# Optimization experiments

Hardware: AMD Instinct MI355X
Metric: run time of the kernel (lower is better)

Reference implementation:

```python
import jax, jax.numpy as jnp
import numpy as np

N = 20000          # num_node
E = 160000         # num edges (avg degree 8)
IN_N = 64          # in_features_node
IN_E = 32          # in_features_edge
HN = 64            # nhid_node
HE = 64            # nhid_edge
KAPPA = 0.9
ITERS = 8          # fixed Picard iterations for the equilibrium solve


def setup_inputs() -> dict:
    key = jax.random.key(0)
    ks = jax.random.split(key, 16)
    f32 = jnp.float32

    def w(k, shape, fan_in):
        return (jax.random.normal(k, shape, dtype=f32) / np.sqrt(fan_in)).astype(f32)

    return {
        # graph structure (int constants)
        "R": jax.random.randint(ks[0], (E,), 0, N),   # receiver node per edge
        "S": jax.random.randint(ks[1], (E,), 0, N),   # sender node per edge
        "H": jax.random.randint(ks[2], (E,), 0, N),   # edge->node aggregation index
        # features (features-first layout, as in the torch code)
        "node_data": jax.random.normal(ks[3], (IN_N, N), dtype=f32),
        "Ra_data": jax.random.normal(ks[4], (IN_E, E), dtype=f32),
        # INECN_Layer parameters
        "W_es": w(ks[5], (HE, HN), HN),      # sender-message weight
        "W_er": w(ks[6], (HE, HN), HN),      # receiver-message weight
        "Omega_e": w(ks[7], (HE, IN_E), IN_E),
        "Wn": w(ks[8], (HN, HN), HN),        # implicit node-state weight
        "Bm": w(ks[9], (HN, HE), HE),        # edge->node mixing
        "Omega_n": w(ks[10], (HN, IN_N), IN_N),
        # dense head (V_0: nhid->nhid, V_1: nhid->in_features_node)
        "V0_w": w(ks[11], (HN, HN), HN),
        "V0_b": jnp.zeros((HN,), dtype=f32),
        "V1_w": w(ks[12], (IN_N, HN), HN),
        "V1_b": jnp.zeros((IN_N,), dtype=f32),
    }


def reference(R, S, H, node_data, Ra_data, W_es, W_er, Omega_e, Wn, Bm,
              Omega_n, V0_w, V0_b, V1_w, V1_b):
    # spectral-norm style contraction: ||kappa * Wn / ||Wn|||| <= kappa (adj_rho = 1)
    Wn_hat = (KAPPA * Wn) / jnp.maximum(jnp.linalg.norm(Wn), 1.0)

    bias_e = Omega_e @ Ra_data        # [HE, E] injected edge features
    bias_n = Omega_n @ node_data      # [HN, N] injected node features

    def step(X, _):
        # edge update: messages from sender/receiver node states
        He_logits = W_es @ X[:, S] + W_er @ X[:, R] + bias_e      # [HE, E]
        He = jax.nn.relu(He_logits)
        # aggregate edge states back to nodes
        agg = jax.ops.segment_sum(He.T, H, num_segments=N).T      # [HE, N] -> [HE, N]
        # implicit node update (contraction => convergent fixed point)
        X_new = jax.nn.relu(Wn_hat @ X + Bm @ agg + bias_n)       # [HN, N]
        return X_new, None

    X0 = jnp.zeros((HN, N), dtype=node_data.dtype)
    X, _ = jax.lax.scan(step, X0, None, length=ITERS)

    # final edge states / logits at the (approximate) fixed point
    He_logits3 = W_es @ X[:, S] + W_er @ X[:, R] + bias_e         # [HE, E]
    He = jax.nn.relu(He_logits3)

    # dense head: x = V_1(dropout(relu(V_0(x.T))))  (eval mode: dropout = identity)
    x = X.T                                                        # [N, HN]
    x = jax.nn.relu(x @ V0_w.T + V0_b)                             # [N, HN]
    x = x @ V1_w.T + V1_b                                          # [N, IN_N]
    return (x, He, He_logits3)
```

## Files before the change

### kernel.cpp

```cpp
#include <hip/hip_runtime.h>
#include <math.h>

#define KAPPA 0.9f
#define ST 68
#define TN 32

__device__ __forceinline__ float relu_f(float v) { return fmaxf(v, 0.0f); }

__global__ __launch_bounds__(256) void wnhat_kernel(const float* __restrict__ Wn,
                                                    float* __restrict__ Wn_hat) {
  __shared__ float red[4];
  int t = threadIdx.x;
  float v[16];
  float s = 0.f;
#pragma unroll
  for (int j = 0; j < 16; ++j) { v[j] = Wn[t + 256 * j]; s += v[j] * v[j]; }
#pragma unroll
  for (int off = 32; off > 0; off >>= 1) s += __shfl_down(s, off, 64);
  if ((t & 63) == 0) red[t >> 6] = s;
  __syncthreads();
  float norm = sqrtf(red[0] + red[1] + red[2] + red[3]);
  float scale = KAPPA / fmaxf(norm, 1.0f);
#pragma unroll
  for (int j = 0; j < 16; ++j) Wn_hat[t + 256 * j] = v[j] * scale;
}

__global__ __launch_bounds__(256) void bias_n_kernel(const float* __restrict__ node_data,
                                                     const float* __restrict__ Om_n,
                                                     float* __restrict__ bias_n, int N) {
  __shared__ float NdT[64][ST];
  __shared__ float Om[64][ST];
  int t = threadIdx.x;
  int n_base = blockIdx.x * 64;
#pragma unroll
  for (int j = 0; j < 16; ++j) {
    int f = t + 256 * j;
    int r = f >> 6, c = f & 63;
    float val = (n_base + c < N) ? node_data[(size_t)r * N + n_base + c] : 0.f;
    NdT[c][r] = val;
    Om[r][c] = Om_n[f];
  }
  __syncthreads();
  int ni = t & 15, h4 = (t >> 4) * 4;
  float acc[4][4] = {};
#pragma unroll 4
  for (int k = 0; k < 64; k += 4) {
    float4 a[4], w[4];
#pragma unroll
    for (int i = 0; i < 4; ++i) a[i] = *(const float4*)&NdT[ni + 16 * i][k];
#pragma unroll
    for (int j = 0; j < 4; ++j) w[j] = *(const float4*)&Om[h4 + j][k];
#pragma unroll
    for (int i = 0; i < 4; ++i)
#pragma unroll
      for (int j = 0; j < 4; ++j)
        acc[i][j] += a[i].x * w[j].x + a[i].y * w[j].y + a[i].z * w[j].z + a[i].w * w[j].w;
  }
#pragma unroll
  for (int i = 0; i < 4; ++i) {
    int n = n_base + ni + 16 * i;
    if (n < N) {
      float4 o = make_float4(acc[i][0], acc[i][1], acc[i][2], acc[i][3]);
      *(float4*)&bias_n[(size_t)n * 64 + h4] = o;
    }
  }
}

__global__ void hist_kernel(const int* __restrict__ H, int* __restrict__ count, int E) {
  int e = blockIdx.x * 256 + threadIdx.x;
  if (e < E) atomicAdd(&count[H[e]], 1);
}

__global__ __launch_bounds__(256) void scan_kernel(int* count, int* row_off, int* cursor,
                                                   int N, int E) {
  __shared__ int offs[256];
  __shared__ int sums[256];
  int t = threadIdx.x;
  int chunk = (N + 255) / 256;
  int lo = t * chunk, hi = min(lo + chunk, N);
  int s = 0;
  for (int n = lo; n < hi; ++n) s += count[n];
  sums[t] = s;
  __syncthreads();
  if (t == 0) {
    int run = 0;
    for (int i = 0; i < 256; ++i) { offs[i] = run; run += sums[i]; }
  }
  __syncthreads();
  int run = offs[t];
  for (int n = lo; n < hi; ++n) {
    int c = count[n];
    row_off[n] = run;
    cursor[n] = run;
    run += c;
  }
  if (t == 0) row_off[N] = E;
}

__global__ void scatter_kernel(const int* __restrict__ H, const int* __restrict__ S,
                               const int* __restrict__ R, int* cursor,
                               int* __restrict__ Ss, int* __restrict__ Rs,
                               int* __restrict__ inv_perm, int E) {
  int e = blockIdx.x * 256 + threadIdx.x;
  if (e < E) {
    int h = H[e];
    int pos = atomicAdd(&cursor[h], 1);
    Ss[pos] = S[e];
    Rs[pos] = R[e];
    inv_perm[e] = pos;
  }
}

__global__ __launch_bounds__(256) void bias_build_kernel(const float* __restrict__ Ra,
                                                         const float* __restrict__ Om_e,
                                                         const int* __restrict__ inv_perm,
                                                         float* __restrict__ bias_s, int E) {
  __shared__ float OmT[64][36];
  __shared__ float RaT[64][36];
  int t = threadIdx.x;
  int e_base = blockIdx.x * 64;
#pragma unroll
  for (int j = 0; j < 8; ++j) {
    int f = t + 256 * j;
    int r = f >> 5, c = f & 31;
    OmT[r][c] = Om_e[f];
  }
#pragma unroll
  for (int j = 0; j < 8; ++j) {
    int f = t + 256 * j;
    int r = f >> 6, c = f & 63;
    int ee = e_base + c;
    RaT[c][r] = (ee < E) ? Ra[(size_t)r * E + ee] : 0.f;
  }
  __syncthreads();
  int ei = t & 15, h4 = (t >> 4) * 4;
  float acc[4][4] = {};
#pragma unroll 4
  for (int jj = 0; jj < 32; jj += 4) {
    float4 ra[4], om[4];
#pragma unroll
    for (int i = 0; i < 4; ++i) ra[i] = *(const float4*)&RaT[ei + 16 * i][jj];
#pragma unroll
    for (int j = 0; j < 4; ++j) om[j] = *(const float4*)&OmT[h4 + j][jj];
#pragma unroll
    for (int i = 0; i < 4; ++i)
#pragma unroll
      for (int j = 0; j < 4; ++j)
        acc[i][j] += ra[i].x * om[j].x + ra[i].y * om[j].y + ra[i].z * om[j].z +
                     ra[i].w * om[j].w;
  }
#pragma unroll
  for (int i = 0; i < 4; ++i) {
    int e = e_base + ei + 16 * i;
    if (e < E) {
      int p = inv_perm[e];
      float4 o = make_float4(acc[i][0], acc[i][1], acc[i][2], acc[i][3]);
      *(float4*)&bias_s[(size_t)p * 64 + h4] = o;
    }
  }
}

template <int FIRST, int LAST>
__global__ __launch_bounds__(256) void iter_kernel(
    const float* __restrict__ X, const float* __restrict__ MS_in,
    const float* __restrict__ MR_in, const float* __restrict__ bias_s,
    const int* __restrict__ Ss, const int* __restrict__ Rs,
    const int* __restrict__ row_off, const float* __restrict__ bias_n,
    const float* __restrict__ Wn_hat, const float* __restrict__ Bm,
    const float* __restrict__ W_es, const float* __restrict__ W_er,
    const float* __restrict__ V0_w, const float* __restrict__ V0_b,
    const float* __restrict__ V1_w, const float* __restrict__ V1_b,
    float* __restrict__ Xout, float* __restrict__ MS_out,
    float* __restrict__ MR_out, float* __restrict__ head_out, int N) {
  __shared__ float Wa[64][ST], Wb[64][ST];
  __shared__ float Xsh[TN][ST], Ash[TN][ST];
  __shared__ float b0s[64], b1s[64];
  int t = threadIdx.x;
  int n_base = blockIdx.x * TN;
#pragma unroll
  for (int j = 0; j < 16; ++j) {
    int f = t + 256 * j;
    int r = f >> 6, c = f & 63;
    Wa[r][c] = Wn_hat[f];
    Wb[r][c] = Bm[f];
  }
  int n8 = t >> 3;
  int q8 = t & 7;
  int nd = n_base + n8;
  bool ok = nd < N;
  if (!FIRST) {
    float4 x0 = make_float4(0, 0, 0, 0), x1 = x0;
    if (ok) {
      x0 = *(const float4*)&X[(size_t)nd * 64 + q8 * 8];
      x1 = *(const float4*)&X[(size_t)nd * 64 + q8 * 8 + 4];
    }
    *(float4*)&Xsh[n8][q8 * 8] = x0;
    *(float4*)&Xsh[n8][q8 * 8 + 4] = x1;
  }
  float4 a0 = make_float4(0, 0, 0, 0), a1 = a0;
  if (ok) {
    int r0 = row_off[nd], r1 = row_off[nd + 1];
    for (int p = r0; p < r1; ++p) {
      const float* bp = &bias_s[(size_t)p * 64 + q8 * 8];
      float4 b0 = *(const float4*)(bp + 0);
      float4 b1 = *(const float4*)(bp + 4);
      if (FIRST) {
        a0.x += relu_f(b0.x); a0.y += relu_f(b0.y); a0.z += relu_f(b0.z); a0.w += relu_f(b0.w);
        a1.x += relu_f(b1.x); a1.y += relu_f(b1.y); a1.z += relu_f(b1.z); a1.w += relu_f(b1.w);
      } else {
        int s = Ss[p], r = Rs[p];
        const float* mp = &MS_in[(size_t)s * 64 + q8 * 8];
        const float* rp = &MR_in[(size_t)r * 64 + q8 * 8];
        float4 m0 = *(const float4*)(mp + 0), m1 = *(const float4*)(mp + 4);
        float4 r0v = *(const float4*)(rp + 0), r1v = *(const float4*)(rp + 4);
        a0.x += relu_f(m0.x + r0v.x + b0.x); a0.y += relu_f(m0.y + r0v.y + b0.y);
        a0.z += relu_f(m0.z + r0v.z + b0.z); a0.w += relu_f(m0.w + r0v.w + b0.w);
        a1.x += relu_f(m1.x + r1v.x + b1.x); a1.y += relu_f(m1.y + r1v.y + b1.y);
        a1.z += relu_f(m1.z + r1v.z + b1.z); a1.w += relu_f(m1.w + r1v.w + b1.w);
      }
    }
  }
  *(float4*)&Ash[n8][q8 * 8] = a0;
  *(float4*)&Ash[n8][q8 * 8 + 4] = a1;
  __syncthreads();
  int ni = t & 15, h4 = (t >> 4) * 4;
  float acc[2][4] = {};
#pragma unroll 4
  for (int k = 0; k < 64; k += 4) {
    float4 xv[2], av[2], wv[4], bv[4];
#pragma unroll
    for (int i = 0; i < 2; ++i) {
      if (!FIRST) xv[i] = *(const float4*)&Xsh[ni + 16 * i][k];
      av[i] = *(const float4*)&Ash[ni + 16 * i][k];
    }
#pragma unroll
    for (int j = 0; j < 4; ++j) {
      wv[j] = *(const float4*)&Wa[h4 + j][k];
      bv[j] = *(const float4*)&Wb[h4 + j][k];
    }
#pragma unroll
    for (int i = 0; i < 2; ++i)
#pragma unroll
      for (int j = 0; j < 4; ++j) {
        float v = av[i].x * bv[j].x + av[i].y * bv[j].y + av[i].z * bv[j].z +
                  av[i].w * bv[j].w;
        if (!FIRST)
          v += xv[i].x * wv[j].x + xv[i].y * wv[j].y + xv[i].z * wv[j].z +
               xv[i].w * wv[j].w;
        acc[i][j] += v;
      }
  }
  __syncthreads();
#pragma unroll
  for (int i = 0; i < 2; ++i) {
    int nn = n_base + ni + 16 * i;
    float4 bb = make_float4(0, 0, 0, 0);
    if (nn < N) bb = *(const float4*)&bias_n[(size_t)nn * 64 + h4];
    float x0 = relu_f(acc[i][0] + bb.x);
    float x1 = relu_f(acc[i][1] + bb.y);
    float x2 = relu_f(acc[i][2] + bb.z);
    float x3 = relu_f(acc[i][3] + bb.w);
    if (!LAST && nn < N)
      *(float4*)&Xout[(size_t)nn * 64 + h4] = make_float4(x0, x1, x2, x3);
    *(float4*)&Xsh[ni + 16 * i][h4] = make_float4(x0, x1, x2, x3);
  }
#pragma unroll
  for (int j = 0; j < 16; ++j) {
    int f = t + 256 * j;
    int r = f >> 6, c = f & 63;
    Wa[r][c] = W_es[f];
    Wb[r][c] = W_er[f];
  }
  __syncthreads();
  {
    float ma[2][4] = {}, ra[2][4] = {};
#pragma unroll 4
    for (int k = 0; k < 64; k += 4) {
      float4 xv[2], ws[4], wr[4];
#pragma unroll
      for (int i = 0; i < 2; ++i) xv[i] = *(const float4*)&Xsh[ni + 16 * i][k];
#pragma unroll
      for (int j = 0; j < 4; ++j) {
        ws[j] = *(const float4*)&Wa[h4 + j][k];
        wr[j] = *(const float4*)&Wb[h4 + j][k];
      }
#pragma unroll
      for (int i = 0; i < 2; ++i)
#pragma unroll
        for (int j = 0; j < 4; ++j) {
          ma[i][j] += xv[i].x * ws[j].x + xv[i].y * ws[j].y + xv[i].z * ws[j].z +
                      xv[i].w * ws[j].w;
          ra[i][j] += xv[i].x * wr[j].x + xv[i].y * wr[j].y + xv[i].z * wr[j].z +
                      xv[i].w * wr[j].w;
        }
    }
#pragma unroll
    for (int i = 0; i < 2; ++i) {
      int nn = n_base + ni + 16 * i;
      if (nn < N) {
        *(float4*)&MS_out[(size_t)nn * 64 + h4] =
            make_float4(ma[i][0], ma[i][1], ma[i][2], ma[i][3]);
        *(float4*)&MR_out[(size_t)nn * 64 + h4] =
            make_float4(ra[i][0], ra[i][1], ra[i][2], ra[i][3]);
      }
    }
  }
  if (LAST) {
    __syncthreads();
#pragma unroll
    for (int j = 0; j < 16; ++j) {
      int f = t + 256 * j;
      int r = f >> 6, c = f & 63;
      Wa[r][c] = V0_w[f];
      Wb[r][c] = V1_w[f];
    }
    if (t < 64) b0s[t] = V0_b[t];
    else if (t < 128) b1s[t - 64] = V1_b[t - 64];
    __syncthreads();
    float c1[2][4] = {};
#pragma unroll 4
    for (int k = 0; k < 64; k += 4) {
      float4 xv[2], wv[4];
#pragma unroll
      for (int i = 0; i < 2; ++i) xv[i] = *(const float4*)&Xsh[ni + 16 * i][k];
#pragma unroll
      for (int j = 0; j < 4; ++j) wv[j] = *(const float4*)&Wa[h4 + j][k];
#pragma unroll
      for (int i = 0; i < 2; ++i)
#pragma unroll
        for (int j = 0; j < 4; ++j)
          c1[i][j] += xv[i].x * wv[j].x + xv[i].y * wv[j].y + xv[i].z * wv[j].z +
                      xv[i].w * wv[j].w;
    }
    __syncthreads();
#pragma unroll
    for (int i = 0; i < 2; ++i) {
      float4 o;
      o.x = relu_f(c1[i][0] + b0s[h4 + 0]);
      o.y = relu_f(c1[i][1] + b0s[h4 + 1]);
      o.z = relu_f(c1[i][2] + b0s[h4 + 2]);
      o.w = relu_f(c1[i][3] + b0s[h4 + 3]);
      *(float4*)&Xsh[ni + 16 * i][h4] = o;
    }
    __syncthreads();
    float c2[2][4] = {};
#pragma unroll 4
    for (int k = 0; k < 64; k += 4) {
      float4 xv[2], wv[4];
#pragma unroll
      for (int i = 0; i < 2; ++i) xv[i] = *(const float4*)&Xsh[ni + 16 * i][k];
#pragma unroll
      for (int j = 0; j < 4; ++j) wv[j] = *(const float4*)&Wb[h4 + j][k];
#pragma unroll
      for (int i = 0; i < 2; ++i)
#pragma unroll
        for (int j = 0; j < 4; ++j)
          c2[i][j] += xv[i].x * wv[j].x + xv[i].y * wv[j].y + xv[i].z * wv[j].z +
                      xv[i].w * wv[j].w;
    }
#pragma unroll
    for (int i = 0; i < 2; ++i) {
      int nn = n_base + ni + 16 * i;
      if (nn < N) {
        float4 o;
        o.x = c2[i][0] + b1s[h4 + 0];
        o.y = c2[i][1] + b1s[h4 + 1];
        o.z = c2[i][2] + b1s[h4 + 2];
        o.w = c2[i][3] + b1s[h4 + 3];
        *(float4*)&head_out[(size_t)nn * 64 + h4] = o;
      }
    }
  }
}

__global__ __launch_bounds__(256) void edge_final_kernel(
    const float* __restrict__ MS, const float* __restrict__ MR,
    const int* __restrict__ S, const int* __restrict__ R,
    const float* __restrict__ Om_e, const float* __restrict__ Ra,
    float* __restrict__ He_out, float* __restrict__ Hel_out, int E) {
  __shared__ float T[64][ST];
  __shared__ float pool2[4608];
  int t = threadIdx.x;
  int e_base = blockIdx.x * 64;
#pragma unroll
  for (int j = 0; j < 8; ++j) {
    int f = t + 256 * j;
    int r = f >> 5, c = f & 31;
    pool2[r * 36 + c] = Om_e[f];
  }
#pragma unroll
  for (int j = 0; j < 8; ++j) {
    int f = t + 256 * j;
    int r = f >> 6, c = f & 63;
    int e2 = e_base + c;
    pool2[2304 + c * 36 + r] = (e2 < E) ? Ra[(size_t)r * E + e2] : 0.f;
  }
  {
    int e = t >> 2, q = t & 3;
    int ee = e_base + e;
    int ec = (ee < E) ? ee : 0;
    int s = S[ec], r = R[ec];
    const float* mp = &MS[(size_t)s * 64 + q * 16];
    const float* rp = &MR[(size_t)r * 64 + q * 16];
#pragma unroll
    for (int c = 0; c < 4; ++c) {
      float4 mv = *(const float4*)(mp + 4 * c);
      float4 rv = *(const float4*)(rp + 4 * c);
      *(float4*)&T[e][q * 16 + 4 * c] =
          make_float4(mv.x + rv.x, mv.y + rv.y, mv.z + rv.z, mv.w + rv.w);
    }
  }
  __syncthreads();
  int ei = t & 15, h4 = (t >> 4) * 4;
  float acc[4][4] = {};
#pragma unroll 4
  for (int jj = 0; jj < 32; jj += 4) {
    float4 ra[4], om[4];
#pragma unroll
    for (int i = 0; i < 4; ++i)
      ra[i] = *(const float4*)&pool2[2304 + (ei + 16 * i) * 36 + jj];
#pragma unroll
    for (int j = 0; j < 4; ++j) om[j] = *(const float4*)&pool2[(h4 + j) * 36 + jj];
#pragma unroll
    for (int i = 0; i < 4; ++i)
#pragma unroll
      for (int j = 0; j < 4; ++j)
        acc[i][j] += ra[i].x * om[j].x + ra[i].y * om[j].y + ra[i].z * om[j].z +
                     ra[i].w * om[j].w;
  }
#pragma unroll
  for (int i = 0; i < 4; ++i) {
    float4 tv = *(const float4*)&T[ei + 16 * i][h4];
    acc[i][0] += tv.x;
    acc[i][1] += tv.y;
    acc[i][2] += tv.z;
    acc[i][3] += tv.w;
  }
  __syncthreads();
#pragma unroll
  for (int i = 0; i < 4; ++i)
#pragma unroll
    for (int j = 0; j < 4; ++j)
      pool2[(ei + 16 * i) * 65 + h4 + j] = acc[i][j];
  __syncthreads();
  {
    int e4 = (t & 15) * 4, h0 = t >> 4;
#pragma unroll
    for (int rep = 0; rep < 4; ++rep) {
      int h = h0 + 16 * rep;
      float4 v;
      v.x = pool2[(e4 + 0) * 65 + h];
      v.y = pool2[(e4 + 1) * 65 + h];
      v.z = pool2[(e4 + 2) * 65 + h];
      v.w = pool2[(e4 + 3) * 65 + h];
      size_t idx = (size_t)h * E + e_base + e4;
      if (e_base + e4 < E) {
        *(float4*)&Hel_out[idx] = v;
        float4 u = make_float4(relu_f(v.x), relu_f(v.y), relu_f(v.z), relu_f(v.w));
        *(float4*)&He_out[idx] = u;
      }
    }
  }
}

extern "C" void kernel_launch(void* const* d_in, const int* in_sizes, int n_in,
                              void* d_out, int out_size, void* d_ws, size_t ws_size,
                              hipStream_t stream) {
  const int* R = (const int*)d_in[0];
  const int* S = (const int*)d_in[1];
  const int* H = (const int*)d_in[2];
  const float* node_data = (const float*)d_in[3];
  const float* Ra = (const float*)d_in[4];
  const float* W_es = (const float*)d_in[5];
  const float* W_er = (const float*)d_in[6];
  const float* Om_e = (const float*)d_in[7];
  const float* Wn = (const float*)d_in[8];
  const float* Bm = (const float*)d_in[9];
  const float* Om_n = (const float*)d_in[10];
  const float* V0_w = (const float*)d_in[11];
  const float* V0_b = (const float*)d_in[12];
  const float* V1_w = (const float*)d_in[13];
  const float* V1_b = (const float*)d_in[14];
  const int E = in_sizes[0];
  const int N = in_sizes[3] / 64;
  const size_t N64 = (size_t)N * 64;

  float* ws = (float*)d_ws;
  float* Wn_hat = ws;
  float* bias_n = Wn_hat + 4096;
  float* X0 = bias_n + N64;
  float* X1p = X0 + N64;
  float* MS_B = X1p + N64;
  float* MR_B = MS_B + N64;
  int* row_off = (int*)(MR_B + N64);
  int* cursor = row_off + (N + 1);
  int* Ss = cursor + N;
  int* Rs = Ss + E;
  int* inv_perm = Rs + E;

  float* out = (float*)d_out;
  float* out_x = out;
  float* out_He = out + N64;
  float* out_Hel = out_He + (size_t)64 * E;
  float* bias_s = out_He;
  float* MS_A = out_Hel;
  float* MR_A = out_Hel + N64;

  int nb_node = (N + 63) / 64;
  int nb_iter = (N + TN - 1) / TN;
  int nb_edge = (E + 63) / 64;
  int nb_flat = (E + 255) / 256;

  hipMemsetAsync(X0, 0, N64 * sizeof(float), stream);
  hipMemsetAsync(cursor, 0, (size_t)N * sizeof(int), stream);
  wnhat_kernel<<<1, 256, 0, stream>>>(Wn, Wn_hat);
  bias_n_kernel<<<nb_node, 256, 0, stream>>>(node_data, Om_n, bias_n, N);
  hist_kernel<<<nb_flat, 256, 0, stream>>>(H, cursor, E);
  scan_kernel<<<1, 256, 0, stream>>>(cursor, row_off, cursor, N, E);
  scatter_kernel<<<nb_flat, 256, 0, stream>>>(H, S, R, cursor, Ss, Rs, inv_perm, E);
  bias_build_kernel<<<nb_edge, 256, 0, stream>>>(Ra, Om_e, inv_perm, bias_s, E);

  float* Xa = X0;
  float* Xb = X1p;
  const float* msi = nullptr;
  const float* mri = nullptr;
  for (int it = 0; it < 8; ++it) {
    float* mso = (it & 1) ? MS_B : MS_A;
    float* mro = (it & 1) ? MR_B : MR_A;
    if (it == 0)
      iter_kernel<1, 0><<<nb_iter, 256, 0, stream>>>(
          Xa, nullptr, nullptr, bias_s, Ss, Rs, row_off, bias_n, Wn_hat, Bm, W_es, W_er,
          V0_w, V0_b, V1_w, V1_b, Xb, mso, mro, out_x, N);
    else if (it < 7)
      iter_kernel<0, 0><<<nb_iter, 256, 0, stream>>>(
          Xa, msi, mri, bias_s, Ss, Rs, row_off, bias_n, Wn_hat, Bm, W_es, W_er,
          V0_w, V0_b, V1_w, V1_b, Xb, mso, mro, out_x, N);
    else
      iter_kernel<0, 1><<<nb_iter, 256, 0, stream>>>(
          Xa, msi, mri, bias_s, Ss, Rs, row_off, bias_n, Wn_hat, Bm, W_es, W_er,
          V0_w, V0_b, V1_w, V1_b, Xb, mso, mro, out_x, N);
    msi = mso;
    mri = mro;
    float* tmp = Xa; Xa = Xb; Xb = tmp;
  }
  edge_final_kernel<<<nb_edge, 256, 0, stream>>>(MS_B, MR_B, S, R, Om_e, Ra,
                                                 out_He, out_Hel, E);
}
```

Before: 459.7 us.

## Drop shared weight staging in iter kernel, halve node tile, read weights from cache

The iteration kernel no longer copies the 64x64 weight matrices into shared memory. Each thread now reads them directly from global memory, relying on L1/L2 caching. The node tile shrinks from 32 to 16 nodes per block, so each thread handles one node and a 4-wide slice of the 64 features. This cuts LDS use and the weight-copy cost per block, which should allow more resident blocks and twice as many blocks for the edge gather. In exchange, weight reads now go through the cache instead of LDS and each block does less register-level reuse. The unneeded X0 memset is also dropped, since the first iteration never reads X.

After: 611.7 us. 1.33x slower.

```diff
diff --git a/kernel.cpp b/kernel.cpp
--- a/kernel.cpp
+++ b/kernel.cpp
@@ -3,7 +3,7 @@
 
 #define KAPPA 0.9f
 #define ST 68
-#define TN 32
+#define TN 16
 
 __device__ __forceinline__ float relu_f(float v) { return fmaxf(v, 0.0f); }
 
@@ -172,203 +172,138 @@
     const float* __restrict__ V1_w, const float* __restrict__ V1_b,
     float* __restrict__ Xout, float* __restrict__ MS_out,
     float* __restrict__ MR_out, float* __restrict__ head_out, int N) {
-  __shared__ float Wa[64][ST], Wb[64][ST];
   __shared__ float Xsh[TN][ST], Ash[TN][ST];
-  __shared__ float b0s[64], b1s[64];
   int t = threadIdx.x;
   int n_base = blockIdx.x * TN;
-#pragma unroll
-  for (int j = 0; j < 16; ++j) {
-    int f = t + 256 * j;
-    int r = f >> 6, c = f & 63;
-    Wa[r][c] = Wn_hat[f];
-    Wb[r][c] = Bm[f];
-  }
-  int n8 = t >> 3;
-  int q8 = t & 7;
-  int nd = n_base + n8;
+  int n16 = t >> 4;
+  int q16 = t & 15;
+  int nd = n_base + n16;
   bool ok = nd < N;
   if (!FIRST) {
-    float4 x0 = make_float4(0, 0, 0, 0), x1 = x0;
-    if (ok) {
-      x0 = *(const float4*)&X[(size_t)nd * 64 + q8 * 8];
-      x1 = *(const float4*)&X[(size_t)nd * 64 + q8 * 8 + 4];
-    }
-    *(float4*)&Xsh[n8][q8 * 8] = x0;
-    *(float4*)&Xsh[n8][q8 * 8 + 4] = x1;
-  }
-  float4 a0 = make_float4(0, 0, 0, 0), a1 = a0;
+    float4 xv = make_float4(0, 0, 0, 0);
+    if (ok) xv = *(const float4*)&X[(size_t)nd * 64 + q16 * 4];
+    *(float4*)&Xsh[n16][q16 * 4] = xv;
+  }
+  float4 a0 = make_float4(0, 0, 0, 0);
   if (ok) {
     int r0 = row_off[nd], r1 = row_off[nd + 1];
     for (int p = r0; p < r1; ++p) {
-      const float* bp = &bias_s[(size_t)p * 64 + q8 * 8];
-      float4 b0 = *(const float4*)(bp + 0);
-      float4 b1 = *(const float4*)(bp + 4);
+      float4 b0 = *(const float4*)&bias_s[(size_t)p * 64 + q16 * 4];
       if (FIRST) {
-        a0.x += relu_f(b0.x); a0.y += relu_f(b0.y); a0.z += relu_f(b0.z); a0.w += relu_f(b0.w);
-        a1.x += relu_f(b1.x); a1.y += relu_f(b1.y); a1.z += relu_f(b1.z); a1.w += relu_f(b1.w);
+        a0.x += relu_f(b0.x); a0.y += relu_f(b0.y);
+        a0.z += relu_f(b0.z); a0.w += relu_f(b0.w);
       } else {
         int s = Ss[p], r = Rs[p];
-        const float* mp = &MS_in[(size_t)s * 64 + q8 * 8];
-        const float* rp = &MR_in[(size_t)r * 64 + q8 * 8];
-        float4 m0 = *(const float4*)(mp + 0), m1 = *(const float4*)(mp + 4);
-        float4 r0v = *(const float4*)(rp + 0), r1v = *(const float4*)(rp + 4);
-        a0.x += relu_f(m0.x + r0v.x + b0.x); a0.y += relu_f(m0.y + r0v.y + b0.y);
-        a0.z += relu_f(m0.z + r0v.z + b0.z); a0.w += relu_f(m0.w + r0v.w + b0.w);
-        a1.x += relu_f(m1.x + r1v.x + b1.x); a1.y += relu_f(m1.y + r1v.y + b1.y);
-        a1.z += relu_f(m1.z + r1v.z + b1.z); a1.w += relu_f(m1.w + r1v.w + b1.w);
+        float4 m0 = *(const float4*)&MS_in[(size_t)s * 64 + q16 * 4];
+        float4 r0v = *(const float4*)&MR_in[(size_t)r * 64 + q16 * 4];
+        a0.x += relu_f(m0.x + r0v.x + b0.x);
+        a0.y += relu_f(m0.y + r0v.y + b0.y);
+        a0.z += relu_f(m0.z + r0v.z + b0.z);
+        a0.w += relu_f(m0.w + r0v.w + b0.w);
       }
     }
   }
-  *(float4*)&Ash[n8][q8 * 8] = a0;
-  *(float4*)&Ash[n8][q8 * 8 + 4] = a1;
+  *(float4*)&Ash[n16][q16 * 4] = a0;
   __syncthreads();
   int ni = t & 15, h4 = (t >> 4) * 4;
-  float acc[2][4] = {};
-#pragma unroll 4
+  float acc[4] = {};
+#pragma unroll 2
   for (int k = 0; k < 64; k += 4) {
-    float4 xv[2], av[2], wv[4], bv[4];
-#pragma unroll
-    for (int i = 0; i < 2; ++i) {
-      if (!FIRST) xv[i] = *(const float4*)&Xsh[ni + 16 * i][k];
-      av[i] = *(const float4*)&Ash[ni + 16 * i][k];
-    }
+    float4 xv, av;
+    if (!FIRST) xv = *(const float4*)&Xsh[ni][k];
+    av = *(const float4*)&Ash[ni][k];
+    float4 wv[4], bv[4];
 #pragma unroll
     for (int j = 0; j < 4; ++j) {
-      wv[j] = *(const float4*)&Wa[h4 + j][k];
-      bv[j] = *(const float4*)&Wb[h4 + j][k];
-    }
-#pragma unroll
-    for (int i = 0; i < 2; ++i)
-#pragma unroll
-      for (int j = 0; j < 4; ++j) {
-        float v = av[i].x * bv[j].x + av[i].y * bv[j].y + av[i].z * bv[j].z +
-                  av[i].w * bv[j].w;
-        if (!FIRST)
-          v += xv[i].x * wv[j].x + xv[i].y * wv[j].y + xv[i].z * wv[j].z +
-               xv[i].w * wv[j].w;
-        acc[i][j] += v;
-      }
-  }
-  __syncthreads();
-#pragma unroll
-  for (int i = 0; i < 2; ++i) {
-    int nn = n_base + ni + 16 * i;
+      if (!FIRST) wv[j] = *(const float4*)&Wn_hat[(size_t)(h4 + j) * 64 + k];
+      bv[j] = *(const float4*)&Bm[(size_t)(h4 + j) * 64 + k];
+    }
+#pragma unroll
+    for (int j = 0; j < 4; ++j) {
+      float v = av.x * bv[j].x + av.y * bv[j].y + av.z * bv[j].z + av.w * bv[j].w;
+      if (!FIRST)
+        v += xv.x * wv[j].x + xv.y * wv[j].y + xv.z * wv[j].z + xv.w * wv[j].w;
+      acc[j] += v;
+    }
+  }
+  __syncthreads();
+  {
+    int nn = n_base + ni;
     float4 bb = make_float4(0, 0, 0, 0);
     if (nn < N) bb = *(const float4*)&bias_n[(size_t)nn * 64 + h4];
-    float x0 = relu_f(acc[i][0] + bb.x);
-    float x1 = relu_f(acc[i][1] + bb.y);
-    float x2 = relu_f(acc[i][2] + bb.z);
-    float x3 = relu_f(acc[i][3] + bb.w);
+    float x0 = relu_f(acc[0] + bb.x);
+    float x1 = relu_f(acc[1] + bb.y);
+    float x2 = relu_f(acc[2] + bb.z);
+    float x3 = relu_f(acc[3] + bb.w);
     if (!LAST && nn < N)
       *(float4*)&Xout[(size_t)nn * 64 + h4] = make_float4(x0, x1, x2, x3);
-    *(float4*)&Xsh[ni + 16 * i][h4] = make_float4(x0, x1, x2, x3);
-  }
-#pragma unroll
-  for (int j = 0; j < 16; ++j) {
-    int f = t + 256 * j;
-    int r = f >> 6, c = f & 63;
-    Wa[r][c] = W_es[f];
-    Wb[r][c] = W_er[f];
+    *(float4*)&Xsh[ni][h4] = make_float4(x0, x1, x2, x3);
   }
   __syncthreads();
   {
-    float ma[2][4] = {}, ra[2][4] = {};
-#pragma unroll 4
+    float ma[4] = {}, ra[4] = {};
+#pragma unroll 2
     for (int k = 0; k < 64; k += 4) {
-      float4 xv[2], ws[4], wr[4];
-#pragma unroll
-      for (int i = 0; i < 2; ++i) xv[i] = *(const float4*)&Xsh[ni + 16 * i][k];
+      float4 xv = *(const float4*)&Xsh[ni][k];
+      float4 ws[4], wr[4];
 #pragma unroll
       for (int j = 0; j < 4; ++j) {
-        ws[j] = *(const float4*)&Wa[h4 + j][k];
-        wr[j] = *(const float4*)&Wb[h4 + j][k];
+        ws[j] = *(const float4*)&W_es[(size_t)(h4 + j) * 64 + k];
+        wr[j] = *(const float4*)&W_er[(size_t)(h4 + j) * 64 + k];
       }
 #pragma unroll
-      for (int i = 0; i < 2; ++i)
-#pragma unroll
-        for (int j = 0; j < 4; ++j) {
-          ma[i][j] += xv[i].x * ws[j].x + xv[i].y * ws[j].y + xv[i].z * ws[j].z +
-                      xv[i].w * ws[j].w;
-          ra[i][j] += xv[i].x * wr[j].x + xv[i].y * wr[j].y + xv[i].z * wr[j].z +
-                      xv[i].w * wr[j].w;
-        }
-    }
-#pragma unroll
-    for (int i = 0; i < 2; ++i) {
-      int nn = n_base + ni + 16 * i;
-      if (nn < N) {
-        *(float4*)&MS_out[(size_t)nn * 64 + h4] =
-            make_float4(ma[i][0], ma[i][1], ma[i][2], ma[i][3]);
-        *(float4*)&MR_out[(size_t)nn * 64 + h4] =
-            make_float4(ra[i][0], ra[i][1], ra[i][2], ra[i][3]);
+      for (int j = 0; j < 4; ++j) {
+        ma[j] += xv.x * ws[j].x + xv.y * ws[j].y + xv.z * ws[j].z + xv.w * ws[j].w;
+        ra[j] += xv.x * wr[j].x + xv.y * wr[j].y + xv.z * wr[j].z + xv.w * wr[j].w;
       }
     }
+    int nn = n_base + ni;
+    if (nn < N) {
+      *(float4*)&MS_out[(size_t)nn * 64 + h4] = make_float4(ma[0], ma[1], ma[2], ma[3]);
+      *(float4*)&MR_out[(size_t)nn * 64 + h4] = make_float4(ra[0], ra[1], ra[2], ra[3]);
+    }
   }
   if (LAST) {
+    float c1[4] = {};
+#pragma unroll 2
+    for (int k = 0; k < 64; k += 4) {
+      float4 xv = *(const float4*)&Xsh[ni][k];
+      float4 wv[4];
+#pragma unroll
+      for (int j = 0; j < 4; ++j) wv[j] = *(const float4*)&V0_w[(size_t)(h4 + j) * 64 + k];
+#pragma unroll
+      for (int j = 0; j < 4; ++j)
+        c1[j] += xv.x * wv[j].x + xv.y * wv[j].y + xv.z * wv[j].z + xv.w * wv[j].w;
+    }
     __syncthreads();
-#pragma unroll
-    for (int j = 0; j < 16; ++j) {
-      int f = t + 256 * j;
-      int r = f >> 6, c = f & 63;
-      Wa[r][c] = V0_w[f];
-      Wb[r][c] = V1_w[f];
-    }
-    if (t < 64) b0s[t] = V0_b[t];
-    else if (t < 128) b1s[t - 64] = V1_b[t - 64];
+    {
+      float4 o;
+      o.x = relu_f(c1[0] + V0_b[h4 + 0]);
+      o.y = relu_f(c1[1] + V0_b[h4 + 1]);
+      o.z = relu_f(c1[2] + V0_b[h4 + 2]);
+      o.w = relu_f(c1[3] + V0_b[h4 + 3]);
+      *(float4*)&Xsh[ni][h4] = o;
+    }
     __syncthreads();
-    float c1[2][4] = {};
-#pragma unroll 4
+    float c2[4] = {};
+#pragma unroll 2
     for (int k = 0; k < 64; k += 4) {
-      float4 xv[2], wv[4];
-#pragma unroll
-      for (int i = 0; i < 2; ++i) xv[i] = *(const float4*)&Xsh[ni + 16 * i][k];
-#pragma unroll
-      for (int j = 0; j < 4; ++j) wv[j] = *(const float4*)&Wa[h4 + j][k];
-#pragma unroll
-      for (int i = 0; i < 2; ++i)
-#pragma unroll
-        for (int j = 0; j < 4; ++j)
-          c1[i][j] += xv[i].x * wv[j].x + xv[i].y * wv[j].y + xv[i].z * wv[j].z +
-                      xv[i].w * wv[j].w;
-    }
-    __syncthreads();
-#pragma unroll
-    for (int i = 0; i < 2; ++i) {
+      float4 xv = *(const float4*)&Xsh[ni][k];
+      float4 wv[4];
+#pragma unroll
+      for (int j = 0; j < 4; ++j) wv[j] = *(const float4*)&V1_w[(size_t)(h4 + j) * 64 + k];
+#pragma unroll
+      for (int j = 0; j < 4; ++j)
+        c2[j] += xv.x * wv[j].x + xv.y * wv[j].y + xv.z * wv[j].z + xv.w * wv[j].w;
+    }
+    int nn = n_base + ni;
+    if (nn < N) {
       float4 o;
-      o.x = relu_f(c1[i][0] + b0s[h4 + 0]);
-      o.y = relu_f(c1[i][1] + b0s[h4 + 1]);
-      o.z = relu_f(c1[i][2] + b0s[h4 + 2]);
-      o.w = relu_f(c1[i][3] + b0s[h4 + 3]);
-      *(float4*)&Xsh[ni + 16 * i][h4] = o;
-    }
-    __syncthreads();
-    float c2[2][4] = {};
-#pragma unroll 4
-    for (int k = 0; k < 64; k += 4) {
-      float4 xv[2], wv[4];
-#pragma unroll
-      for (int i = 0; i < 2; ++i) xv[i] = *(const float4*)&Xsh[ni + 16 * i][k];
-#pragma unroll
-      for (int j = 0; j < 4; ++j) wv[j] = *(const float4*)&Wb[h4 + j][k];
-#pragma unroll
-      for (int i = 0; i < 2; ++i)
-#pragma unroll
-        for (int j = 0; j < 4; ++j)
-          c2[i][j] += xv[i].x * wv[j].x + xv[i].y * wv[j].y + xv[i].z * wv[j].z +
-                      xv[i].w * wv[j].w;
-    }
-#pragma unroll
-    for (int i = 0; i < 2; ++i) {
-      int nn = n_base + ni + 16 * i;
-      if (nn < N) {
-        float4 o;
-        o.x = c2[i][0] + b1s[h4 + 0];
-        o.y = c2[i][1] + b1s[h4 + 1];
-        o.z = c2[i][2] + b1s[h4 + 2];
-        o.w = c2[i][3] + b1s[h4 + 3];
-        *(float4*)&head_out[(size_t)nn * 64 + h4] = o;
-      }
+      o.x = c2[0] + V1_b[h4 + 0];
+      o.y = c2[1] + V1_b[h4 + 1];
+      o.z = c2[2] + V1_b[h4 + 2];
+      o.w = c2[3] + V1_b[h4 + 3];
+      *(float4*)&head_out[(size_t)nn * 64 + h4] = o;
     }
   }
 }
@@ -511,7 +446,6 @@
   int nb_edge = (E + 63) / 64;
   int nb_flat = (E + 255) / 256;
 
-  hipMemsetAsync(X0, 0, N64 * sizeof(float), stream);
   hipMemsetAsync(cursor, 0, (size_t)N * sizeof(int), stream);
   wnhat_kernel<<<1, 256, 0, stream>>>(Wn, Wn_hat);
   bias_n_kernel<<<nb_node, 256, 0, stream>>>(node_data, Om_n, bias_n, N);
```
